# Kernel tuning notes

Hardware: AMD Instinct MI355X
Metric: run time of the kernel (lower is better)

The kernel has to match this reference:

```python
import jax, jax.numpy as jnp
import numpy as np

B, N, D, STK_TOTAL = 8, 2048, 128, 4000


def setup_inputs() -> dict:
    key = jax.random.key(0)
    k1, k2, k3, k4 = jax.random.split(key, 4)
    x = jax.random.normal(k1, (B, N, D), dtype=jnp.float32)
    stk_ten = jax.random.randint(k2, (B, N), 0, STK_TOTAL, dtype=jnp.int32)
    # learned parameter tables (trained state; original inits: ones / xavier-uniform)
    stk_matrix = jax.random.normal(k3, (STK_TOTAL, STK_TOTAL), dtype=jnp.float32)
    stk_weight = jax.random.normal(k4, (STK_TOTAL, STK_TOTAL), dtype=jnp.float32)
    return {"x": x, "stk_ten": stk_ten, "stk_matrix": stk_matrix, "stk_weight": stk_weight}


def reference(x, stk_ten, stk_matrix, stk_weight):
    # x: [B, N, D]; stk_ten: [B, N] int ids < STK_TOTAL
    idx = stk_ten.astype(jnp.int32)
    # per-batch double gather -> [B, N, N] submatrices (vectorized index_select x2)
    M = stk_matrix[idx[:, :, None], idx[:, None, :]]          # [B, N, N]
    W = jnp.abs(stk_weight[idx[:, :, None], idx[:, None, :]])  # [B, N, N]
    n = idx.shape[1]
    eye = jnp.eye(n, dtype=bool)                               # diag removal mask
    M = jnp.where(eye, jnp.float32(0.0), M)                    # stk_m_s - diag_embed(diag)
    W = jnp.where(eye, jnp.float32(0.0), W)
    # dropout is identity in inference mode (training=False)
    att = jax.nn.softmax(W, axis=2)                            # [B, N, N]
    out = jnp.matmul(M * att, x)                               # [B, N, D]
    return out
```

## Files before the change

### kernel.cpp

```cpp
#include <hip/hip_runtime.h>
#include <hip/hip_fp16.h>
#include <math.h>

#define BATCH 8
#define N 2048
#define D 128
#define ST 4000

#define TJ 64
#define IT 16
#define KQ 4
#define TPW 8

typedef short bf16x8 __attribute__((ext_vector_type(8)));
typedef float f32x4  __attribute__((ext_vector_type(4)));
typedef unsigned short u16x4 __attribute__((ext_vector_type(4)));

__device__ __forceinline__ unsigned short f2bf(float f) {
    union { float f; unsigned u; } v; v.f = f;
    const unsigned r = v.u + 0x7FFFu + ((v.u >> 16) & 1u);
    return (unsigned short)(r >> 16);
}

__global__ __launch_bounds__(1024) void sort_kernel(
    const int* __restrict__ stk_ten,
    int* __restrict__ sval,
    int* __restrict__ spos,
    unsigned short* __restrict__ cntT)
{
    __shared__ int hist[4000];
    __shared__ int base[4000];
    __shared__ int wsum[16];
    const int b = blockIdx.x, t = threadIdx.x;
    const int lane = t & 63, wv = t >> 6;
    const int* idxb = stk_ten + b * N;

    for (int j = t; j < 4000; j += 1024) hist[j] = 0;
    __syncthreads();
    const int v0 = idxb[t], v1 = idxb[t + 1024];
    atomicAdd(&hist[v0], 1);
    atomicAdd(&hist[v1], 1);
    __syncthreads();

    for (int j = t; j < 4000; j += 1024) cntT[(size_t)j * 8 + b] = (unsigned short)hist[j];

    int h[4], c[4], run = 0;
    #pragma unroll
    for (int i = 0; i < 4; ++i) {
        const int bi = 4 * t + i;
        h[i] = (bi < 4000) ? hist[bi] : 0;
        run += h[i];
        c[i] = run;
    }
    const int tsum = run;
    int incl = tsum;
    #pragma unroll
    for (int d = 1; d < 64; d <<= 1) {
        const int tmp = __shfl_up(incl, d, 64);
        if (lane >= d) incl += tmp;
    }
    if (lane == 63) wsum[wv] = incl;
    __syncthreads();
    if (t < 16) {
        const int v = wsum[t];
        int iv = v;
        #pragma unroll
        for (int d = 1; d < 16; d <<= 1) {
            const int tmp = __shfl_up(iv, d, 64);
            if (lane >= d) iv += tmp;
        }
        wsum[t] = iv - v;
    }
    __syncthreads();
    const int ex = incl - tsum + wsum[wv];
    #pragma unroll
    for (int i = 0; i < 4; ++i) {
        const int bi = 4 * t + i;
        if (bi < 4000) base[bi] = ex + c[i] - h[i];
    }
    __syncthreads();
    for (int j = t; j < 4000; j += 1024) hist[j] = 0;
    __syncthreads();
    {
        const int p0 = base[v0] + atomicAdd(&hist[v0], 1);
        sval[b * N + p0] = v0; spos[b * N + p0] = t;
        const int p1 = base[v1] + atomicAdd(&hist[v1], 1);
        sval[b * N + p1] = v1; spos[b * N + p1] = t + 1024;
    }
}

__global__ __launch_bounds__(256) void pack_kernel(
    const float* __restrict__ M, const float* __restrict__ W,
    const unsigned short* __restrict__ cntT,
    unsigned short* __restrict__ P2,
    float* __restrict__ Lb)
{
    __shared__ float redL[4][8];
    __shared__ float ediag_s;
    const int r = blockIdx.x;
    const int t = threadIdx.x;
    const int lane = t & 63, wv = t >> 6;
    const size_t rowo = (size_t)r * ST;

    float acc8[8];
    #pragma unroll
    for (int b = 0; b < 8; ++b) acc8[b] = 0.0f;

    for (int it = 0; it < 4; ++it) {
        const int c4 = (t + 256 * it) * 4;
        if (c4 < ST) {
            const f32x4 m4 = __builtin_nontemporal_load((const f32x4*)(M + rowo + c4));
            const f32x4 w4 = __builtin_nontemporal_load((const f32x4*)(W + rowo + c4));
            u16x4 o;
            #pragma unroll
            for (int k = 0; k < 4; ++k) {
                const float e = __expf(fabsf(w4[k]));
                o[k] = f2bf(m4[k] * e);
                if (c4 + k == r) ediag_s = e;
                const uint4 cv = *(const uint4*)(cntT + (size_t)(c4 + k) * 8);
                acc8[0] += (float)(cv.x & 0xFFFFu) * e;
                acc8[1] += (float)(cv.x >> 16)     * e;
                acc8[2] += (float)(cv.y & 0xFFFFu) * e;
                acc8[3] += (float)(cv.y >> 16)     * e;
                acc8[4] += (float)(cv.z & 0xFFFFu) * e;
                acc8[5] += (float)(cv.z >> 16)     * e;
                acc8[6] += (float)(cv.w & 0xFFFFu) * e;
                acc8[7] += (float)(cv.w >> 16)     * e;
            }
            *(u16x4*)(P2 + rowo + c4) = o;
        }
    }

    #pragma unroll
    for (int b = 0; b < 8; ++b) {
        float v = acc8[b];
        #pragma unroll
        for (int d = 1; d < 64; d <<= 1) v += __shfl_xor(v, d, 64);
        if (lane == 0) redL[wv][b] = v;
    }
    __syncthreads();
    if (t < 8) {
        const float s = redL[0][t] + redL[1][t] + redL[2][t] + redL[3][t];
        Lb[(size_t)t * ST + r] = s - ediag_s + 1.0f;
    }
}

__global__ __launch_bounds__(256) void xt_kernel(
    const float* __restrict__ x,
    const int* __restrict__ spos,
    unsigned short* __restrict__ xT)
{
    __shared__ float xs[TJ][129];
    __shared__ int sp_s[TJ];
    const int t  = threadIdx.x;
    const int b  = blockIdx.x >> 5;
    const int jt = blockIdx.x & 31;
    const int j0 = jt * TJ;
    if (t < TJ) sp_s[t] = spos[b * N + j0 + t];
    __syncthreads();
    const int tx = t & 31, ty = t >> 5;
    const float* xb = x + (size_t)b * N * D;
    #pragma unroll
    for (int p = 0; p < 8; ++p) {
        const int r = ty + 8 * p;
        const float* src = xb + (size_t)sp_s[r] * D;
        #pragma unroll
        for (int i = 0; i < 4; ++i)
            xs[r][tx + 32 * i] = src[tx + 32 * i];
    }
    __syncthreads();
    const int jp = t & 31, dd0 = t >> 5;
    unsigned short* xTb = xT + (size_t)b * D * N;
    #pragma unroll
    for (int q = 0; q < 16; ++q) {
        const int dd = dd0 + 8 * q;
        const unsigned lo = f2bf(xs[2 * jp][dd]);
        const unsigned hi = f2bf(xs[2 * jp + 1][dd]);
        *(unsigned*)(xTb + (size_t)dd * N + j0 + 2 * jp) = (hi << 16) | lo;
    }
}

__global__ __launch_bounds__(256) void fused_kernel(
    const unsigned short* __restrict__ xT,
    const int* __restrict__ stk_ten,
    const unsigned short* __restrict__ P2,
    const int* __restrict__ sval,
    const int* __restrict__ spos,
    const float* __restrict__ Lb,
    float* __restrict__ out)
{
    __shared__ __align__(16) unsigned short cs[KQ][IT * 72];
    __shared__ float accs[IT][132];
    __shared__ int ri_s[IT];

    const int t    = threadIdx.x;
    const int lane = t & 63;
    const int w    = t >> 6;
    const int wg   = (blockIdx.x & 7) * 128 + (blockIdx.x >> 3);
    const int b    = wg >> 7;
    const int i0   = (wg & 127) * IT;

    if (t < IT) ri_s[t] = stk_ten[b * N + i0 + t];
    for (int z = t; z < IT * 132; z += 256) (&accs[0][0])[z] = 0.0f;
    __syncthreads();

    unsigned rowbase[IT];
    #pragma unroll
    for (int m = 0; m < IT; ++m) rowbase[m] = (unsigned)ri_s[m] * ST;

    const int* svb = sval + b * N;
    const int* spb = spos + b * N;
    const unsigned short* xTb = xT + (size_t)b * D * N;
    unsigned short* csw = &cs[w][0];

    f32x4 acc[8];
    #pragma unroll
    for (int nb = 0; nb < 8; ++nb)
        #pragma unroll
        for (int r = 0; r < 4; ++r) acc[nb][r] = 0.0f;

    const int jbase = w * (TPW * TJ);
    const int brow  = lane & 15;
    const int bcol  = (lane >> 4) * 8;

    int cj = svb[jbase + lane];
    int pj = spb[jbase + lane];
    unsigned gv[IT];
    #pragma unroll
    for (int m = 0; m < IT; ++m) gv[m] = P2[rowbase[m] + (unsigned)cj];

    for (int tt = 0; tt < TPW; ++tt) {
        const int j0  = jbase + tt * TJ;
        const int j0n = (tt == TPW - 1) ? jbase : j0 + TJ;

        const int cjn = svb[j0n + lane];
        const int pjn = spb[j0n + lane];
        uint4 bv[8];
        #pragma unroll
        for (int nb = 0; nb < 8; ++nb)
            bv[nb] = *(const uint4*)(xTb + (size_t)(nb * 16 + brow) * N + j0 + bcol);

        #pragma unroll
        for (int m = 0; m < IT; ++m) {
            const bool diag = (pj == i0 + m);
            csw[m * 72 + lane] = diag ? (unsigned short)0 : (unsigned short)gv[m];
        }

        const bf16x8 av0 = *(const bf16x8*)(csw + brow * 72 + bcol);
        const bf16x8 av1 = *(const bf16x8*)(csw + brow * 72 + 32 + bcol);

        unsigned gvn[IT];
        #pragma unroll
        for (int m = 0; m < IT; ++m) gvn[m] = P2[rowbase[m] + (unsigned)cjn];

        #pragma unroll
        for (int nb = 0; nb < 8; ++nb)
            acc[nb] = __builtin_amdgcn_mfma_f32_16x16x32_bf16(
                av0, *(const bf16x8*)&bv[nb], acc[nb], 0, 0, 0);
        #pragma unroll
        for (int nb = 0; nb < 8; ++nb)
            bv[nb] = *(const uint4*)(xTb + (size_t)(nb * 16 + brow) * N + j0 + 32 + bcol);
        #pragma unroll
        for (int nb = 0; nb < 8; ++nb)
            acc[nb] = __builtin_amdgcn_mfma_f32_16x16x32_bf16(
                av1, *(const bf16x8*)&bv[nb], acc[nb], 0, 0, 0);

        #pragma unroll
        for (int m = 0; m < IT; ++m) gv[m] = gvn[m];
        cj = cjn; pj = pjn;
    }

    #pragma unroll
    for (int nb = 0; nb < 8; ++nb)
        #pragma unroll
        for (int r = 0; r < 4; ++r)
            atomicAdd(&accs[(lane >> 4) * 4 + r][nb * 16 + (lane & 15)], acc[nb][r]);
    __syncthreads();

    #pragma unroll
    for (int rr = 0; rr < 4; ++rr) {
        const int row = 4 * w + rr;
        const float linv = 1.0f / Lb[(size_t)b * ST + ri_s[row]];
        #pragma unroll
        for (int p = 0; p < 2; ++p) {
            const int dd = lane + 64 * p;
            out[((size_t)(b * N + i0 + row) << 7) + dd] = accs[row][dd] * linv;
        }
    }
}

extern "C" void kernel_launch(void* const* d_in, const int* in_sizes, int n_in,
                              void* d_out, int out_size, void* d_ws, size_t ws_size,
                              hipStream_t stream) {
    const float* x          = (const float*)d_in[0];
    const int*   stk_ten    = (const int*)d_in[1];
    const float* stk_matrix = (const float*)d_in[2];
    const float* stk_weight = (const float*)d_in[3];
    float* out = (float*)d_out;

    unsigned short* P2 = (unsigned short*)d_ws;
    int* sval = (int*)(P2 + (size_t)ST * ST);
    int* spos = sval + BATCH * N;
    unsigned short* cntT = (unsigned short*)(spos + BATCH * N);
    float* Lb = (float*)(cntT + ST * 8);
    unsigned short* xT = (unsigned short*)(Lb + BATCH * ST);

    sort_kernel<<<BATCH, 1024, 0, stream>>>(stk_ten, sval, spos, cntT);
    xt_kernel<<<BATCH * (N / TJ), 256, 0, stream>>>(x, spos, xT);
    pack_kernel<<<ST, 256, 0, stream>>>(stk_matrix, stk_weight, cntT, P2, Lb);
    fused_kernel<<<BATCH * (N / IT), 256, 0, stream>>>(
        xT, stk_ten, P2, sval, spos, Lb, out);
}
```

Measured before the change: 293.0 us.

## Prefetch P2 gathers directly into LDS with double-buffered global_load_lds

Replaces register-held per-lane P2 gathers with asynchronous global_load_lds into a double-buffered per-wave LDS staging area. Gathers are issued two tiles ahead and the wait uses an explicit vmcnt threshold, so gather latency should overlap the MFMA work. Both halves of the x tile are loaded up front, and the accumulation buffer shares a union with the staging area to save LDS. The cost is manual waitcnt reasoning, a 4-byte aligned load with a shift to pick the right 16-bit half, and extra barriers at the end.

```diff
diff --git a/kernel.cpp b/kernel.cpp
--- a/kernel.cpp
+++ b/kernel.cpp
@@ -189,8 +189,13 @@
     const float* __restrict__ Lb,
     float* __restrict__ out)
 {
-    __shared__ __align__(16) unsigned short cs[KQ][IT * 72];
-    __shared__ float accs[IT][132];
+    __shared__ union SMem {
+        struct {
+            unsigned short cs[KQ][IT * 72];
+            unsigned       pg[KQ][2][IT * 64];
+        } lp;
+        float accs[IT][132];
+    } sm;
     __shared__ int ri_s[IT];
 
     const int t    = threadIdx.x;
@@ -201,17 +206,17 @@
     const int i0   = (wg & 127) * IT;
 
     if (t < IT) ri_s[t] = stk_ten[b * N + i0 + t];
-    for (int z = t; z < IT * 132; z += 256) (&accs[0][0])[z] = 0.0f;
-    __syncthreads();
-
-    unsigned rowbase[IT];
-    #pragma unroll
-    for (int m = 0; m < IT; ++m) rowbase[m] = (unsigned)ri_s[m] * ST;
+    __syncthreads();
+
+    unsigned rowoff[IT];
+    #pragma unroll
+    for (int m = 0; m < IT; ++m) rowoff[m] = (unsigned)ri_s[m] * ST;
 
     const int* svb = sval + b * N;
     const int* spb = spos + b * N;
     const unsigned short* xTb = xT + (size_t)b * D * N;
-    unsigned short* csw = &cs[w][0];
+    unsigned short* csw = &sm.lp.cs[w][0];
+    unsigned* pgw = &sm.lp.pg[w][0][0];
 
     f32x4 acc[8];
     #pragma unroll
@@ -223,58 +228,75 @@
     const int brow  = lane & 15;
     const int bcol  = (lane >> 4) * 8;
 
-    int cj = svb[jbase + lane];
-    int pj = spb[jbase + lane];
-    unsigned gv[IT];
-    #pragma unroll
-    for (int m = 0; m < IT; ++m) gv[m] = P2[rowbase[m] + (unsigned)cj];
-
+    int cj  = svb[jbase + lane];
+    int pj  = spb[jbase + lane];
+    int cjn = svb[jbase + TJ + lane];
+    int pjn = spb[jbase + TJ + lane];
+    #pragma unroll
+    for (int m = 0; m < IT; ++m)
+        __builtin_amdgcn_global_load_lds(
+            (const unsigned*)(P2 + rowoff[m] + ((unsigned)cj & ~1u)),
+            pgw + m * 64, 4, 0, 0);
+
+    int buf = 0;
     for (int tt = 0; tt < TPW; ++tt) {
-        const int j0  = jbase + tt * TJ;
-        const int j0n = (tt == TPW - 1) ? jbase : j0 + TJ;
-
-        const int cjn = svb[j0n + lane];
-        const int pjn = spb[j0n + lane];
-        uint4 bv[8];
+        const int j0 = jbase + tt * TJ;
+        const int j2 = (tt + 2 < TPW) ? j0 + 2 * TJ : jbase;
+
+        uint4 bv0[8], bv1[8];
         #pragma unroll
         for (int nb = 0; nb < 8; ++nb)
-            bv[nb] = *(const uint4*)(xTb + (size_t)(nb * 16 + brow) * N + j0 + bcol);
-
+            bv0[nb] = *(const uint4*)(xTb + (size_t)(nb * 16 + brow) * N + j0 + bcol);
+        #pragma unroll
+        for (int nb = 0; nb < 8; ++nb)
+            bv1[nb] = *(const uint4*)(xTb + (size_t)(nb * 16 + brow) * N + j0 + 32 + bcol);
+
+        unsigned* pgn = pgw + (buf ^ 1) * (IT * 64);
+        #pragma unroll
+        for (int m = 0; m < IT; ++m)
+            __builtin_amdgcn_global_load_lds(
+                (const unsigned*)(P2 + rowoff[m] + ((unsigned)cjn & ~1u)),
+                pgn + m * 64, 4, 0, 0);
+
+        asm volatile("s_waitcnt vmcnt(32)" ::: "memory");
+        __builtin_amdgcn_sched_barrier(0);
+
+        const int cj2 = svb[j2 + lane];
+        const int pj2 = spb[j2 + lane];
+
+        const unsigned sh = ((unsigned)cj & 1u) << 4;
+        const unsigned* pgr = pgw + buf * (IT * 64);
         #pragma unroll
         for (int m = 0; m < IT; ++m) {
+            const unsigned u = pgr[m * 64 + lane];
             const bool diag = (pj == i0 + m);
-            csw[m * 72 + lane] = diag ? (unsigned short)0 : (unsigned short)gv[m];
+            csw[m * 72 + lane] = diag ? (unsigned short)0
+                                      : (unsigned short)((u >> sh) & 0xFFFFu);
         }
 
         const bf16x8 av0 = *(const bf16x8*)(csw + brow * 72 + bcol);
         const bf16x8 av1 = *(const bf16x8*)(csw + brow * 72 + 32 + bcol);
 
-        unsigned gvn[IT];
-        #pragma unroll
-        for (int m = 0; m < IT; ++m) gvn[m] = P2[rowbase[m] + (unsigned)cjn];
-
         #pragma unroll
         for (int nb = 0; nb < 8; ++nb)
             acc[nb] = __builtin_amdgcn_mfma_f32_16x16x32_bf16(
-                av0, *(const bf16x8*)&bv[nb], acc[nb], 0, 0, 0);
-        #pragma unroll
-        for (int nb = 0; nb < 8; ++nb)
-            bv[nb] = *(const uint4*)(xTb + (size_t)(nb * 16 + brow) * N + j0 + 32 + bcol);
+                av0, *(const bf16x8*)&bv0[nb], acc[nb], 0, 0, 0);
         #pragma unroll
         for (int nb = 0; nb < 8; ++nb)
             acc[nb] = __builtin_amdgcn_mfma_f32_16x16x32_bf16(
-                av1, *(const bf16x8*)&bv[nb], acc[nb], 0, 0, 0);
-
-        #pragma unroll
-        for (int m = 0; m < IT; ++m) gv[m] = gvn[m];
-        cj = cjn; pj = pjn;
-    }
-
+                av1, *(const bf16x8*)&bv1[nb], acc[nb], 0, 0, 0);
+
+        buf ^= 1; cj = cjn; pj = pjn; cjn = cj2; pjn = pj2;
+    }
+
+    __syncthreads();
+    for (int z = t; z < IT * 132; z += 256) (&sm.accs[0][0])[z] = 0.0f;
+    __syncthreads();
     #pragma unroll
     for (int nb = 0; nb < 8; ++nb)
         #pragma unroll
         for (int r = 0; r < 4; ++r)
-            atomicAdd(&accs[(lane >> 4) * 4 + r][nb * 16 + (lane & 15)], acc[nb][r]);
+            atomicAdd(&sm.accs[(lane >> 4) * 4 + r][nb * 16 + (lane & 15)], acc[nb][r]);
     __syncthreads();
 
     #pragma unroll
@@ -284,7 +306,7 @@
         #pragma unroll
         for (int p = 0; p < 2; ++p) {
             const int dd = lane + 64 * p;
-            out[((size_t)(b * N + i0 + row) << 7) + dd] = accs[row][dd] * linv;
+            out[((size_t)(b * N + i0 + row) << 7) + dd] = sm.accs[row][dd] * linv;
         }
     }
 }
```

Result: slower. 303.4 us (+3.5%).
